# Optimization experiments

Measured on AMD Instinct MI355X. Metric: run time of the kernel, lower is better.

Reference implementation:

```python
import math
import jax, jax.numpy as jnp
import numpy as np

EPS_ATTN = 1e-8
LN_EPS = 1e-5


def layer_norm(x, g, b):
    mu = jnp.mean(x, axis=-1, keepdims=True)
    var = jnp.var(x, axis=-1, keepdims=True)
    return (x - mu) * jax.lax.rsqrt(var + LN_EPS) * g + b


def setup_inputs() -> dict:
    key = jax.random.key(0)
    ks = jax.random.split(key, 12)
    b, n, dim = 8, 8192, 384
    emb = 384
    m = int(emb * 0.5)  # 192 random features
    s = 0.02
    x = jax.random.normal(ks[0], (b, n, dim), dtype=jnp.float32)
    # fixed random-feature matrix (orthogonal*sqrt(m) in torch; random gaussian suffices as a baseline param)
    w = jax.random.normal(ks[1], (m, emb), dtype=jnp.float32) * math.sqrt(m) / math.sqrt(emb)
    # linear weights stored as [in, out] (torch Linear applies x @ W.T + b)
    kqv_w = jax.random.normal(ks[2], (dim, 3 * emb), dtype=jnp.float32) * s
    kqv_b = jax.random.normal(ks[3], (3 * emb,), dtype=jnp.float32) * s
    proj_w = jax.random.normal(ks[4], (emb, emb), dtype=jnp.float32) * s
    proj_b = jax.random.normal(ks[5], (emb,), dtype=jnp.float32) * s
    ln1_g = 1.0 + jax.random.normal(ks[6], (dim,), dtype=jnp.float32) * s
    ln1_b = jax.random.normal(ks[7], (dim,), dtype=jnp.float32) * s
    ln2_g = 1.0 + jax.random.normal(ks[8], (emb,), dtype=jnp.float32) * s
    ln2_b = jax.random.normal(ks[9], (emb,), dtype=jnp.float32) * s
    mlp_w1 = jax.random.normal(ks[10], (emb, emb), dtype=jnp.float32) * s
    mlp_b1 = jnp.zeros((emb,), dtype=jnp.float32)
    mlp_w2 = jax.random.normal(ks[11], (emb, emb), dtype=jnp.float32) * s
    mlp_b2 = jnp.zeros((emb,), dtype=jnp.float32)
    return {"x": x, "w": w, "kqv_w": kqv_w, "kqv_b": kqv_b, "proj_w": proj_w,
            "proj_b": proj_b, "ln1_g": ln1_g, "ln1_b": ln1_b, "ln2_g": ln2_g,
            "ln2_b": ln2_b, "mlp_w1": mlp_w1, "mlp_b1": mlp_b1,
            "mlp_w2": mlp_w2, "mlp_b2": mlp_b2}


def prm_exp(x, w):
    # FAVOR+ positive random features: exp(w @ x - |x|^2/2) / sqrt(m)
    m = w.shape[0]
    xd = 0.5 * jnp.sum(x * x, axis=-1, keepdims=True)          # [b, t, 1]
    wtx = jnp.einsum('bti,mi->btm', x, w)                       # [b, t, m]
    return jnp.exp(wtx - xd) / math.sqrt(m)


def reference(x, w, kqv_w, kqv_b, proj_w, proj_b, ln1_g, ln1_b,
              ln2_g, ln2_b, mlp_w1, mlp_b1, mlp_w2, mlp_b2):
    emb = proj_w.shape[0]
    h = layer_norm(x, ln1_g, ln1_b)
    kqv = h @ kqv_w + kqv_b                                     # [b, n, 3*emb]
    k, q, v = jnp.split(kqv, 3, axis=-1)
    kp = prm_exp(k, w)                                          # [b, n, m]
    qp = prm_exp(q, w)                                          # [b, n, m]
    D = jnp.einsum('btm,bm->bt', qp, kp.sum(axis=1))[..., None] # [b, n, 1]
    kptv = jnp.einsum('btn,btm->bnm', v, kp)                    # [b, emb, m]
    y = jnp.einsum('btm,bnm->btn', qp, kptv) / (D + EPS_ATTN)   # [b, n, emb]
    y = v + (y @ proj_w + proj_b)                               # residual (dropout=0)
    h2 = layer_norm(y, ln2_g, ln2_b)
    mlp = jax.nn.gelu(h2 @ mlp_w1 + mlp_b1, approximate=False) @ mlp_w2 + mlp_b2
    return y + mlp
```

## Files before the change

### kernel.cpp

```cpp
#include <hip/hip_runtime.h>
#include <cstdint>
#include <cstddef>


typedef __attribute__((ext_vector_type(8))) short s16x8;
typedef __attribute__((ext_vector_type(4))) short s16x4;
typedef __attribute__((ext_vector_type(4))) float fx4;
typedef __attribute__((ext_vector_type(8))) float fx8;

__device__ __forceinline__ float bf2f(short s) {
  union { float f; unsigned u; } z; z.u = ((unsigned)(unsigned short)s) << 16; return z.f;
}
__device__ __forceinline__ short f2bf(float f) {
  union { float f; unsigned u; } z; z.f = f;
  unsigned u = z.u;
  u += 0x7fffu + ((u >> 16) & 1u);
  return (short)(u >> 16);
}

__device__ __forceinline__ void mfma_bf16(fx4& d, s16x8 a, s16x8 b) {
  asm("v_mfma_f32_16x16x32_bf16 %0, %1, %2, %0" : "+v"(d) : "v"(a), "v"(b));
}

enum : int { M_BIAS=1, M_EXP=2, M_DIV=4, M_RESID=8, M_GELU=16, M_TSTORE=32,
             M_BATCHBT=64, M_KQVT=128, M_RESIDT=256, M_F32OUT=512,
             M_XA=1024, M_DOTB=2048 };

template<int BM, int BN, int MODE>
__global__ __launch_bounds__(256)
void gemm_tn(const short* __restrict__ A, int lda,
             const short* __restrict__ Bt, int ldbt, long btStride,
             short* __restrict__ C, int ldc,
             int K,
             const float* __restrict__ bias,
             const float* __restrict__ rowvec, float escale,
             const short* __restrict__ resid, int ldr, int rcol,
             short* __restrict__ vt)
{
  constexpr int WM = BM / 2, WN = BN / 2, MR = WM / 16, NR = WN / 16;
  constexpr int AIT = BM * 8 / 256, BIT = BN * 8 / 256;
  __shared__ __align__(16) short Al[BM][64];
  __shared__ __align__(16) short Bl[BN][64];
  __shared__ float xdl[(MODE & (M_XA | M_DOTB)) ? BM : 1];

  const int tid = threadIdx.x;
  const int gx = gridDim.x;
  const int nwg = gx * gridDim.y;
  const int o = blockIdx.x + gx * blockIdx.y;
  const int swz = (o & 7) * (nwg >> 3) + (o >> 3);
  const int bx = swz % gx, by = swz / gx;
  const int row0 = by * BM, col0 = bx * BN;

  const short* Bt2 = (MODE & M_BATCHBT)
      ? Bt + (size_t)(row0 >> 13) * (size_t)btStride : Bt;
  const int w = tid >> 6, l = tid & 63;
  const int wr = w >> 1, wc = w & 1;
  const int lr = l & 15, lk = l >> 4;

  fx4 acc[MR][NR];
#pragma unroll
  for (int m = 0; m < MR; ++m)
#pragma unroll
    for (int n = 0; n < NR; ++n)
#pragma unroll
      for (int j = 0; j < 4; ++j) acc[m][n][j] = 0.0f;

  s16x8 areg[AIT], breg[BIT];
  float xacc[(MODE & (M_XA | M_DOTB)) ? AIT : 1];
#pragma unroll
  for (int i = 0; i < (int)(sizeof(xacc) / sizeof(float)); ++i) xacc[i] = 0.0f;

  auto loadA = [&](int kt) {
    const short* p = A + (size_t)row0 * lda + kt * 64;
#pragma unroll
    for (int i = 0; i < AIT; ++i) {
      int ch = i * 256 + tid;
      areg[i] = *(const s16x8*)(p + (size_t)(ch >> 3) * lda + ((ch & 7) * 8));
      if (MODE & M_XA) {
#pragma unroll
        for (int jj = 0; jj < 8; ++jj) { float f = bf2f(areg[i][jj]); xacc[i] += f * f; }
      }
      if (MODE & M_DOTB) {
        const float* dv = rowvec + (row0 >> 13) * 192 + kt * 64 + (ch & 7) * 8;
#pragma unroll
        for (int jj = 0; jj < 8; ++jj) xacc[i] += bf2f(areg[i][jj]) * dv[jj];
      }
    }
  };
  auto loadB = [&](int kt) {
    const short* p = Bt2 + (size_t)col0 * ldbt + kt * 64;
#pragma unroll
    for (int i = 0; i < BIT; ++i) {
      int ch = i * 256 + tid;
      breg[i] = *(const s16x8*)(p + (size_t)(ch >> 3) * ldbt + ((ch & 7) * 8));
    }
  };
  auto storeA = [&]() {
#pragma unroll
    for (int i = 0; i < AIT; ++i) {
      int ch = i * 256 + tid, row = ch >> 3;
      *(s16x8*)&Al[row][((ch ^ row) & 7) * 8] = areg[i];
    }
  };
  auto storeB = [&]() {
#pragma unroll
    for (int i = 0; i < BIT; ++i) {
      int ch = i * 256 + tid, row = ch >> 3;
      *(s16x8*)&Bl[row][((ch ^ row) & 7) * 8] = breg[i];
    }
  };

  const int NT = K / 64;
  loadA(0); loadB(0); storeA(); storeB();
  __syncthreads();
  for (int kt = 0; kt < NT; ++kt) {
    if (kt + 1 < NT) { loadA(kt + 1); loadB(kt + 1); }
#pragma unroll
    for (int kk = 0; kk < 2; ++kk) {
      s16x8 af[MR], bfr[NR];
#pragma unroll
      for (int m = 0; m < MR; ++m) {
        const int ar = wr * WM + m * 16 + lr;
        af[m] = *(const s16x8*)&Al[ar][(((kk * 4 + lk) ^ ar) & 7) * 8];
      }
#pragma unroll
      for (int n = 0; n < NR; ++n) {
        const int br = wc * WN + n * 16 + lr;
        bfr[n] = *(const s16x8*)&Bl[br][(((kk * 4 + lk) ^ br) & 7) * 8];
      }
#pragma unroll
      for (int m = 0; m < MR; ++m)
#pragma unroll
        for (int n = 0; n < NR; ++n)
          mfma_bf16(acc[m][n], af[m], bfr[n]);
    }
    if (kt + 1 < NT) {
      __syncthreads();
      storeA(); storeB();
      __syncthreads();
    }
  }

  if (MODE & (M_XA | M_DOTB)) {
#pragma unroll
    for (int i = 0; i < (int)(sizeof(xacc) / sizeof(float)); ++i) {
      float s = xacc[i];
      s += __shfl_xor(s, 1); s += __shfl_xor(s, 2); s += __shfl_xor(s, 4);
      if ((tid & 7) == 0) xdl[i * 32 + (tid >> 3)] = (MODE & M_XA) ? 0.5f * s : s;
    }
    __syncthreads();
  }

#pragma unroll
  for (int m = 0; m < MR; ++m) {
#pragma unroll
    for (int n = 0; n < NR; ++n) {
      const int gcol = col0 + wc * WN + n * 16 + lr;
      const float bv = (MODE & M_BIAS) ? bias[gcol] : 0.0f;
#pragma unroll
      for (int j = 0; j < 4; ++j) {
        const int lrow = wr * WM + m * 16 + lk * 4 + j;
        const int grow = row0 + lrow;
        float v = acc[m][n][j] + bv;
        if (MODE & M_EXP)  v = expf(v - xdl[lrow]) * escale;
        if (MODE & M_DIV)  v = v / (xdl[lrow] + 1e-8f);
        if (MODE & M_GELU) v = 0.5f * v * (1.0f + erff(v * 0.70710678118654752f));
        if (MODE & M_RESID)  v += bf2f(resid[(size_t)grow * ldr + rcol + gcol]);
        if (MODE & M_RESIDT) v += bf2f(resid[((size_t)((grow >> 13) * ldr + gcol)) * 8192 + (grow & 8191)]);
        if (MODE & M_F32OUT) {
          ((float*)C)[(size_t)grow * ldc + gcol] = v;
        } else if (MODE & M_TSTORE) {
          C[((size_t)((grow >> 13) * ldc + gcol)) * 8192 + (grow & 8191)] = f2bf(v);
        } else if (MODE & M_KQVT) {
          if (gcol < 768) C[(size_t)grow * 768 + gcol] = f2bf(v);
          else vt[((size_t)((grow >> 13) * 384 + (gcol - 768))) * 8192 + (grow & 8191)] = f2bf(v);
        } else {
          C[(size_t)grow * ldc + gcol] = f2bf(v);
        }
      }
    }
  }
}

__global__ __launch_bounds__(256)
void gemm_kptv(const short* __restrict__ vT, const short* __restrict__ kpT,
               float* __restrict__ part)
{
  __shared__ __align__(16) short Al[128][64];
  __shared__ __align__(16) short Bl[64][64];
  const int tid = threadIdx.x;
  const int b = blockIdx.z >> 3, s = blockIdx.z & 7;
  const int row0 = blockIdx.x * 128, col0 = blockIdx.y * 64;
  const short* A  = vT  + ((size_t)(b * 384 + row0)) * 8192 + s * 1024;
  const short* Bt = kpT + ((size_t)(b * 192 + col0)) * 8192 + s * 1024;
  const int w = tid >> 6, l = tid & 63;
  const int wr = w >> 1, wc = w & 1, lr = l & 15, lk = l >> 4;

  fx4 acc[4][2];
#pragma unroll
  for (int m = 0; m < 4; ++m)
#pragma unroll
    for (int n = 0; n < 2; ++n)
#pragma unroll
      for (int j = 0; j < 4; ++j) acc[m][n][j] = 0.0f;

  s16x8 areg[4], breg[2];
  auto loadA = [&](int kt) {
#pragma unroll
    for (int i = 0; i < 4; ++i) {
      int ch = i * 256 + tid;
      areg[i] = *(const s16x8*)(A + kt * 64 + (size_t)(ch >> 3) * 8192 + ((ch & 7) * 8));
    }
  };
  auto loadB = [&](int kt) {
#pragma unroll
    for (int i = 0; i < 2; ++i) {
      int ch = i * 256 + tid;
      breg[i] = *(const s16x8*)(Bt + kt * 64 + (size_t)(ch >> 3) * 8192 + ((ch & 7) * 8));
    }
  };
  auto storeA = [&]() {
#pragma unroll
    for (int i = 0; i < 4; ++i) {
      int ch = i * 256 + tid, row = ch >> 3;
      *(s16x8*)&Al[row][((ch ^ row) & 7) * 8] = areg[i];
    }
  };
  auto storeB = [&]() {
#pragma unroll
    for (int i = 0; i < 2; ++i) {
      int ch = i * 256 + tid, row = ch >> 3;
      *(s16x8*)&Bl[row][((ch ^ row) & 7) * 8] = breg[i];
    }
  };

  loadA(0); loadB(0); storeA(); storeB();
  __syncthreads();
  for (int kt = 0; kt < 16; ++kt) {
    if (kt + 1 < 16) { loadA(kt + 1); loadB(kt + 1); }
#pragma unroll
    for (int kk = 0; kk < 2; ++kk) {
      s16x8 af[4], bfr[2];
#pragma unroll
      for (int m = 0; m < 4; ++m) {
        const int ar = wr * 64 + m * 16 + lr;
        af[m] = *(const s16x8*)&Al[ar][(((kk * 4 + lk) ^ ar) & 7) * 8];
      }
#pragma unroll
      for (int n = 0; n < 2; ++n) {
        const int br = wc * 32 + n * 16 + lr;
        bfr[n] = *(const s16x8*)&Bl[br][(((kk * 4 + lk) ^ br) & 7) * 8];
      }
#pragma unroll
      for (int m = 0; m < 4; ++m)
#pragma unroll
        for (int n = 0; n < 2; ++n)
          mfma_bf16(acc[m][n], af[m], bfr[n]);
    }
    if (kt + 1 < 16) {
      __syncthreads();
      storeA(); storeB();
      __syncthreads();
    }
  }

  float* outp = part + (size_t)blockIdx.z * 73728;
#pragma unroll
  for (int m = 0; m < 4; ++m)
#pragma unroll
    for (int n = 0; n < 2; ++n) {
      const int gm = col0 + wc * 32 + n * 16 + lr;
#pragma unroll
      for (int j = 0; j < 4; ++j) {
        const int gn = row0 + wr * 64 + m * 16 + lk * 4 + j;
        outp[(size_t)gn * 192 + gm] = acc[m][n][j];
      }
    }
}

__global__ void kptv_reduce(const float* __restrict__ part, short* __restrict__ outb)
{
  const int i = blockIdx.x * 256 + threadIdx.x;
  const int b = i / 73728, j = i - b * 73728;
  const float* p = part + (size_t)b * 8 * 73728 + j;
  float s = 0.0f;
#pragma unroll
  for (int k = 0; k < 8; ++k) s += p[(size_t)k * 73728];
  outb[i] = f2bf(s);
}

template<typename T>
__global__ __launch_bounds__(256)
void ln_kernel(const T* __restrict__ in, const float* __restrict__ g,
               const float* __restrict__ bta, short* __restrict__ out)
{
  const int tid = threadIdx.x, w = tid >> 6, l = tid & 63;
  const size_t t = (size_t)blockIdx.x * 4 + w;
  float x[8]; float sum = 0.0f, ss = 0.0f;
  const bool act = l < 48;
  if (act) {
    if constexpr (sizeof(T) == 2) {
      s16x8 v = *(const s16x8*)((const short*)in + t * 384 + l * 8);
#pragma unroll
      for (int i = 0; i < 8; ++i) x[i] = bf2f(v[i]);
    } else {
      fx8 v = *(const fx8*)((const float*)in + t * 384 + l * 8);
#pragma unroll
      for (int i = 0; i < 8; ++i) x[i] = v[i];
    }
#pragma unroll
    for (int i = 0; i < 8; ++i) { sum += x[i]; ss += x[i] * x[i]; }
  }
#pragma unroll
  for (int d = 1; d < 64; d <<= 1) { sum += __shfl_xor(sum, d); ss += __shfl_xor(ss, d); }
  const float mu = sum * (1.0f / 384.0f);
  const float rs = rsqrtf(ss * (1.0f / 384.0f) - mu * mu + 1e-5f);
  if (act) {
    fx8 gv = *(const fx8*)(g + l * 8);
    fx8 bv = *(const fx8*)(bta + l * 8);
    s16x8 o;
#pragma unroll
    for (int i = 0; i < 8; ++i) o[i] = f2bf((x[i] - mu) * rs * gv[i] + bv[i]);
    *(s16x8*)(out + t * 384 + l * 8) = o;
  }
}

__global__ __launch_bounds__(256)
void rowsum_kernel(const short* __restrict__ kpT, float* __restrict__ sum)
{
  const int tid = threadIdx.x;
  const short* row = kpT + (size_t)blockIdx.x * 8192;
  float s = 0.0f;
  for (int i = tid; i < 1024; i += 256) {
    s16x8 v = ((const s16x8*)row)[i];
#pragma unroll
    for (int k = 0; k < 8; ++k) s += bf2f(v[k]);
  }
#pragma unroll
  for (int d = 1; d < 64; d <<= 1) s += __shfl_xor(s, d);
  __shared__ float ps[4];
  if ((tid & 63) == 0) ps[tid >> 6] = s;
  __syncthreads();
  if (tid == 0) sum[blockIdx.x] = ps[0] + ps[1] + ps[2] + ps[3];
}

__global__ void transpose_kernel(const float* __restrict__ src, short* __restrict__ dst,
                                 int R, int Cc)
{
  __shared__ float tile[32][33];
  const int c0 = blockIdx.x * 32, r0 = blockIdx.y * 32;
  for (int i = threadIdx.y; i < 32; i += 8)
    tile[i][threadIdx.x] = src[(size_t)(r0 + i) * Cc + c0 + threadIdx.x];
  __syncthreads();
  for (int i = threadIdx.y; i < 32; i += 8)
    dst[(size_t)(c0 + i) * R + r0 + threadIdx.x] = f2bf(tile[threadIdx.x][i]);
}

__global__ void convert_kernel(const float* __restrict__ src, short* __restrict__ dst)
{
  const int i = blockIdx.x * 1024 + threadIdx.x * 4;
  fx4 v = *(const fx4*)(src + i);
  s16x4 o;
#pragma unroll
  for (int k = 0; k < 4; ++k) o[k] = f2bf(v[k]);
  *(s16x4*)(dst + i) = o;
}

extern "C" void kernel_launch(void* const* d_in, const int* in_sizes, int n_in,
                              void* d_out, int out_size, void* d_ws, size_t ws_size,
                              hipStream_t stream)
{
  const float* x      = (const float*)d_in[0];
  const float* w      = (const float*)d_in[1];
  const float* kqv_w  = (const float*)d_in[2];
  const float* kqv_b  = (const float*)d_in[3];
  const float* proj_w = (const float*)d_in[4];
  const float* proj_b = (const float*)d_in[5];
  const float* ln1_g  = (const float*)d_in[6];
  const float* ln1_b  = (const float*)d_in[7];
  const float* ln2_g  = (const float*)d_in[8];
  const float* ln2_b  = (const float*)d_in[9];
  const float* w1     = (const float*)d_in[10];
  const float* b1     = (const float*)d_in[11];
  const float* w2     = (const float*)d_in[12];
  const float* b2     = (const float*)d_in[13];

  char* p = (char*)d_ws;
  auto take = [&](size_t n) { char* r = p; p += (n + 255) & ~(size_t)255; return r; };
  short* wtKQV  = (short*)take(1152 * 384 * 2);
  short* wtPROJ = (short*)take(384 * 384 * 2);
  short* wtM1   = (short*)take(384 * 384 * 2);
  short* wtM2   = (short*)take(384 * 384 * 2);
  short* wB     = (short*)take(192 * 384 * 2);
  short* KQ     = (short*)take((size_t)65536 * 768 * 2);
  short* VT     = (short*)take((size_t)8 * 384 * 8192 * 2);
  char*  KPQ    = take(50331648);
  float* KPSUM = (float*)take(1536 * 4);
  float* KPART = (float*)take((size_t)64 * 73728 * 4);
  short* KPTVB = (short*)take(1179648);

  short* H   = (short*)KPQ;
  short* KPT = (short*)KPQ;
  short* QP  = (short*)(KPQ + 25165824);
  short* Y   = (short*)KPQ;
  short* YA  = KQ;
  short* G   = KQ;
  short* H2  = VT;

  const float ESC = 0.07216878364870323f;
  dim3 blk(256);

  transpose_kernel<<<dim3(36, 12), dim3(32, 8), 0, stream>>>(kqv_w, wtKQV, 384, 1152);
  transpose_kernel<<<dim3(12, 12), dim3(32, 8), 0, stream>>>(proj_w, wtPROJ, 384, 384);
  transpose_kernel<<<dim3(12, 12), dim3(32, 8), 0, stream>>>(w1, wtM1, 384, 384);
  transpose_kernel<<<dim3(12, 12), dim3(32, 8), 0, stream>>>(w2, wtM2, 384, 384);
  convert_kernel<<<72, blk, 0, stream>>>(w, wB);

  ln_kernel<float><<<16384, blk, 0, stream>>>(x, ln1_g, ln1_b, H);

  gemm_tn<128, 128, M_BIAS | M_KQVT><<<dim3(9, 512), blk, 0, stream>>>(
      H, 384, wtKQV, 384, 0, KQ, 768, 384, kqv_b, nullptr, 0.f, nullptr, 0, 0, VT);

  gemm_tn<128, 64, M_EXP | M_TSTORE | M_XA><<<dim3(3, 512), blk, 0, stream>>>(
      KQ, 768, wB, 384, 0, KPT, 192, 384, nullptr, nullptr, ESC, nullptr, 0, 0, nullptr);
  gemm_tn<128, 64, M_EXP | M_XA><<<dim3(3, 512), blk, 0, stream>>>(
      KQ + 384, 768, wB, 384, 0, QP, 192, 384, nullptr, nullptr, ESC, nullptr, 0, 0, nullptr);

  rowsum_kernel<<<1536, blk, 0, stream>>>(KPT, KPSUM);

  gemm_kptv<<<dim3(3, 3, 64), blk, 0, stream>>>(VT, KPT, KPART);
  kptv_reduce<<<2304, blk, 0, stream>>>(KPART, KPTVB);

  gemm_tn<128, 128, M_DIV | M_BATCHBT | M_DOTB><<<dim3(3, 512), blk, 0, stream>>>(
      QP, 192, KPTVB, 192, 73728, YA, 384, 192, nullptr, KPSUM, 0.f, nullptr, 0, 0, nullptr);

  gemm_tn<128, 128, M_BIAS | M_RESIDT><<<dim3(3, 512), blk, 0, stream>>>(
      YA, 384, wtPROJ, 384, 0, Y, 384, 384, proj_b, nullptr, 0.f, VT, 384, 0, nullptr);

  ln_kernel<short><<<16384, blk, 0, stream>>>(Y, ln2_g, ln2_b, H2);

  gemm_tn<128, 128, M_BIAS | M_GELU><<<dim3(3, 512), blk, 0, stream>>>(
      H2, 384, wtM1, 384, 0, G, 384, 384, b1, nullptr, 0.f, nullptr, 0, 0, nullptr);

  gemm_tn<128, 128, M_BIAS | M_RESID | M_F32OUT><<<dim3(3, 512), blk, 0, stream>>>(
      G, 384, wtM2, 384, 0, (short*)d_out, 384, 384, b2, nullptr, 0.f, Y, 384, 0, nullptr);
}
```

Baseline: 486.4 us.

## Use direct global-to-LDS async loads with double-buffered tiles in GEMMs

Adds an async mode to the tiled GEMM that uses global_load_lds to copy A/B tiles straight from global memory into double-buffered LDS, with the XOR swizzle moved to the global address side. This drops the register staging and the extra barrier-bounded store phase, so the next tile's load can overlap the current tile's MFMA work with one barrier per K step. It is enabled for the KQV, projection and two MLP GEMMs. It doubles LDS use per block, which may lower occupancy, and it relies on the barrier also waiting for the outstanding LDS-direct loads.

```diff
diff --git a/kernel.cpp b/kernel.cpp
--- a/kernel.cpp
+++ b/kernel.cpp
@@ -22,9 +22,15 @@
   asm("v_mfma_f32_16x16x32_bf16 %0, %1, %2, %0" : "+v"(d) : "v"(a), "v"(b));
 }
 
+__device__ __forceinline__ void gload_lds16(const short* src, short* lds) {
+  __builtin_amdgcn_global_load_lds(
+      (const __attribute__((address_space(1))) unsigned int*)src,
+      (__attribute__((address_space(3))) unsigned int*)lds, 16, 0, 0);
+}
+
 enum : int { M_BIAS=1, M_EXP=2, M_DIV=4, M_RESID=8, M_GELU=16, M_TSTORE=32,
              M_BATCHBT=64, M_KQVT=128, M_RESIDT=256, M_F32OUT=512,
-             M_XA=1024, M_DOTB=2048 };
+             M_XA=1024, M_DOTB=2048, M_ASYNC=4096 };
 
 template<int BM, int BN, int MODE>
 __global__ __launch_bounds__(256)
@@ -37,10 +43,12 @@
              const short* __restrict__ resid, int ldr, int rcol,
              short* __restrict__ vt)
 {
+  constexpr bool ASYNC = (MODE & M_ASYNC) != 0;
+  constexpr int NB = ASYNC ? 2 : 1;
   constexpr int WM = BM / 2, WN = BN / 2, MR = WM / 16, NR = WN / 16;
   constexpr int AIT = BM * 8 / 256, BIT = BN * 8 / 256;
-  __shared__ __align__(16) short Al[BM][64];
-  __shared__ __align__(16) short Bl[BN][64];
+  __shared__ __align__(16) short Al[NB][BM][64];
+  __shared__ __align__(16) short Bl[NB][BN][64];
   __shared__ float xdl[(MODE & (M_XA | M_DOTB)) ? BM : 1];
 
   const int tid = threadIdx.x;
@@ -99,34 +107,59 @@
 #pragma unroll
     for (int i = 0; i < AIT; ++i) {
       int ch = i * 256 + tid, row = ch >> 3;
-      *(s16x8*)&Al[row][((ch ^ row) & 7) * 8] = areg[i];
+      *(s16x8*)&Al[0][row][((ch ^ row) & 7) * 8] = areg[i];
     }
   };
   auto storeB = [&]() {
 #pragma unroll
     for (int i = 0; i < BIT; ++i) {
       int ch = i * 256 + tid, row = ch >> 3;
-      *(s16x8*)&Bl[row][((ch ^ row) & 7) * 8] = breg[i];
+      *(s16x8*)&Bl[0][row][((ch ^ row) & 7) * 8] = breg[i];
+    }
+  };
+
+  auto stageA = [&](int buf, int kt) {
+    const short* pb = A + (size_t)row0 * lda + kt * 64;
+#pragma unroll
+    for (int i = 0; i < AIT; ++i) {
+      int ch = i * 256 + tid, row = ch >> 3, c = ch & 7;
+      gload_lds16(pb + (size_t)row * lda + ((c ^ row) & 7) * 8,
+                  (short*)Al + (size_t)buf * BM * 64 + ch * 8);
+    }
+  };
+  auto stageB = [&](int buf, int kt) {
+    const short* pb = Bt2 + (size_t)col0 * ldbt + kt * 64;
+#pragma unroll
+    for (int i = 0; i < BIT; ++i) {
+      int ch = i * 256 + tid, row = ch >> 3, c = ch & 7;
+      gload_lds16(pb + (size_t)row * ldbt + ((c ^ row) & 7) * 8,
+                  (short*)Bl + (size_t)buf * BN * 64 + ch * 8);
     }
   };
 
   const int NT = K / 64;
-  loadA(0); loadB(0); storeA(); storeB();
+  int buf = 0;
+  if constexpr (ASYNC) { stageA(0, 0); stageB(0, 0); }
+  else { loadA(0); loadB(0); storeA(); storeB(); }
   __syncthreads();
   for (int kt = 0; kt < NT; ++kt) {
-    if (kt + 1 < NT) { loadA(kt + 1); loadB(kt + 1); }
+    if constexpr (ASYNC) {
+      if (kt + 1 < NT) { stageA(buf ^ 1, kt + 1); stageB(buf ^ 1, kt + 1); }
+    } else {
+      if (kt + 1 < NT) { loadA(kt + 1); loadB(kt + 1); }
+    }
 #pragma unroll
     for (int kk = 0; kk < 2; ++kk) {
       s16x8 af[MR], bfr[NR];
 #pragma unroll
       for (int m = 0; m < MR; ++m) {
         const int ar = wr * WM + m * 16 + lr;
-        af[m] = *(const s16x8*)&Al[ar][(((kk * 4 + lk) ^ ar) & 7) * 8];
+        af[m] = *(const s16x8*)&Al[buf][ar][(((kk * 4 + lk) ^ ar) & 7) * 8];
       }
 #pragma unroll
       for (int n = 0; n < NR; ++n) {
         const int br = wc * WN + n * 16 + lr;
-        bfr[n] = *(const s16x8*)&Bl[br][(((kk * 4 + lk) ^ br) & 7) * 8];
+        bfr[n] = *(const s16x8*)&Bl[buf][br][(((kk * 4 + lk) ^ br) & 7) * 8];
       }
 #pragma unroll
       for (int m = 0; m < MR; ++m)
@@ -134,10 +167,15 @@
         for (int n = 0; n < NR; ++n)
           mfma_bf16(acc[m][n], af[m], bfr[n]);
     }
-    if (kt + 1 < NT) {
+    if constexpr (ASYNC) {
       __syncthreads();
-      storeA(); storeB();
-      __syncthreads();
+      buf ^= 1;
+    } else {
+      if (kt + 1 < NT) {
+        __syncthreads();
+        storeA(); storeB();
+        __syncthreads();
+      }
     }
   }
 
@@ -418,7 +456,7 @@
 
   ln_kernel<float><<<16384, blk, 0, stream>>>(x, ln1_g, ln1_b, H);
 
-  gemm_tn<128, 128, M_BIAS | M_KQVT><<<dim3(9, 512), blk, 0, stream>>>(
+  gemm_tn<128, 128, M_BIAS | M_KQVT | M_ASYNC><<<dim3(9, 512), blk, 0, stream>>>(
       H, 384, wtKQV, 384, 0, KQ, 768, 384, kqv_b, nullptr, 0.f, nullptr, 0, 0, VT);
 
   gemm_tn<128, 64, M_EXP | M_TSTORE | M_XA><<<dim3(3, 512), blk, 0, stream>>>(
@@ -434,14 +472,14 @@
   gemm_tn<128, 128, M_DIV | M_BATCHBT | M_DOTB><<<dim3(3, 512), blk, 0, stream>>>(
       QP, 192, KPTVB, 192, 73728, YA, 384, 192, nullptr, KPSUM, 0.f, nullptr, 0, 0, nullptr);
 
-  gemm_tn<128, 128, M_BIAS | M_RESIDT><<<dim3(3, 512), blk, 0, stream>>>(
+  gemm_tn<128, 128, M_BIAS | M_RESIDT | M_ASYNC><<<dim3(3, 512), blk, 0, stream>>>(
       YA, 384, wtPROJ, 384, 0, Y, 384, 384, proj_b, nullptr, 0.f, VT, 384, 0, nullptr);
 
   ln_kernel<short><<<16384, blk, 0, stream>>>(Y, ln2_g, ln2_b, H2);
 
-  gemm_tn<128, 128, M_BIAS | M_GELU><<<dim3(3, 512), blk, 0, stream>>>(
+  gemm_tn<128, 128, M_BIAS | M_GELU | M_ASYNC><<<dim3(3, 512), blk, 0, stream>>>(
       H2, 384, wtM1, 384, 0, G, 384, 384, b1, nullptr, 0.f, nullptr, 0, 0, nullptr);
 
-  gemm_tn<128, 128, M_BIAS | M_RESID | M_F32OUT><<<dim3(3, 512), blk, 0, stream>>>(
+  gemm_tn<128, 128, M_BIAS | M_RESID | M_F32OUT | M_ASYNC><<<dim3(3, 512), blk, 0, stream>>>(
       G, 384, wtM2, 384, 0, (short*)d_out, 384, 384, b2, nullptr, 0.f, Y, 384, 0, nullptr);
 }
```

After: 501.5 us. +3.1%, slower.

## Stage GEMM epilogue through shared memory for coalesced vectorized stores

Applied to the files above, without the earlier changes.

Replaces per-element scalar global stores in the GEMM epilogue with a staging pass through LDS. The LDS is reused via a union with the A/B tiles, with a swizzle for transposed outputs. Each half (or quarter for fp32 output) of the tile is written to LDS and then stored to global memory as 16-byte vectors, including the transposed layouts used for V and the kp/qp outputs. This removes the strided 2-byte writes, especially the transposed ones, at the cost of extra barriers and LDS traffic.

```diff
diff --git a/kernel.cpp b/kernel.cpp
--- a/kernel.cpp
+++ b/kernel.cpp
@@ -39,8 +39,13 @@
 {
   constexpr int WM = BM / 2, WN = BN / 2, MR = WM / 16, NR = WN / 16;
   constexpr int AIT = BM * 8 / 256, BIT = BN * 8 / 256;
-  __shared__ __align__(16) short Al[BM][64];
-  __shared__ __align__(16) short Bl[BN][64];
+  constexpr int PITCH = BN + 8;
+
+  __shared__ __align__(16) union UB {
+    struct { short Al[BM][64]; short Bl[BN][64]; } s;
+    short b16[64 * PITCH];
+    float b32[32 * PITCH];
+  } u;
   __shared__ float xdl[(MODE & (M_XA | M_DOTB)) ? BM : 1];
 
   const int tid = threadIdx.x;
@@ -99,14 +104,14 @@
 #pragma unroll
     for (int i = 0; i < AIT; ++i) {
       int ch = i * 256 + tid, row = ch >> 3;
-      *(s16x8*)&Al[row][((ch ^ row) & 7) * 8] = areg[i];
+      *(s16x8*)&u.s.Al[row][((ch ^ row) & 7) * 8] = areg[i];
     }
   };
   auto storeB = [&]() {
 #pragma unroll
     for (int i = 0; i < BIT; ++i) {
       int ch = i * 256 + tid, row = ch >> 3;
-      *(s16x8*)&Bl[row][((ch ^ row) & 7) * 8] = breg[i];
+      *(s16x8*)&u.s.Bl[row][((ch ^ row) & 7) * 8] = breg[i];
     }
   };
 
@@ -121,12 +126,12 @@
 #pragma unroll
       for (int m = 0; m < MR; ++m) {
         const int ar = wr * WM + m * 16 + lr;
-        af[m] = *(const s16x8*)&Al[ar][(((kk * 4 + lk) ^ ar) & 7) * 8];
+        af[m] = *(const s16x8*)&u.s.Al[ar][(((kk * 4 + lk) ^ ar) & 7) * 8];
       }
 #pragma unroll
       for (int n = 0; n < NR; ++n) {
         const int br = wc * WN + n * 16 + lr;
-        bfr[n] = *(const s16x8*)&Bl[br][(((kk * 4 + lk) ^ br) & 7) * 8];
+        bfr[n] = *(const s16x8*)&u.s.Bl[br][(((kk * 4 + lk) ^ br) & 7) * 8];
       }
 #pragma unroll
       for (int m = 0; m < MR; ++m)
@@ -142,6 +147,7 @@
   }
 
   if (MODE & (M_XA | M_DOTB)) {
+    __syncthreads();
 #pragma unroll
     for (int i = 0; i < (int)(sizeof(xacc) / sizeof(float)); ++i) {
       float s = xacc[i];
@@ -151,32 +157,91 @@
     __syncthreads();
   }
 
-#pragma unroll
-  for (int m = 0; m < MR; ++m) {
-#pragma unroll
-    for (int n = 0; n < NR; ++n) {
-      const int gcol = col0 + wc * WN + n * 16 + lr;
-      const float bv = (MODE & M_BIAS) ? bias[gcol] : 0.0f;
-#pragma unroll
-      for (int j = 0; j < 4; ++j) {
-        const int lrow = wr * WM + m * 16 + lk * 4 + j;
-        const int grow = row0 + lrow;
-        float v = acc[m][n][j] + bv;
-        if (MODE & M_EXP)  v = expf(v - xdl[lrow]) * escale;
-        if (MODE & M_DIV)  v = v / (xdl[lrow] + 1e-8f);
-        if (MODE & M_GELU) v = 0.5f * v * (1.0f + erff(v * 0.70710678118654752f));
-        if (MODE & M_RESID)  v += bf2f(resid[(size_t)grow * ldr + rcol + gcol]);
-        if (MODE & M_RESIDT) v += bf2f(resid[((size_t)((grow >> 13) * ldr + gcol)) * 8192 + (grow & 8191)]);
-        if (MODE & M_F32OUT) {
-          ((float*)C)[(size_t)grow * ldc + gcol] = v;
-        } else if (MODE & M_TSTORE) {
-          C[((size_t)((grow >> 13) * ldc + gcol)) * 8192 + (grow & 8191)] = f2bf(v);
-        } else if (MODE & M_KQVT) {
-          if (gcol < 768) C[(size_t)grow * 768 + gcol] = f2bf(v);
-          else vt[((size_t)((grow >> 13) * 384 + (gcol - 768))) * 8192 + (grow & 8191)] = f2bf(v);
-        } else {
-          C[(size_t)grow * ldc + gcol] = f2bf(v);
+  auto val = [&](int m, int n, int j) -> float {
+    const int gcol = col0 + wc * WN + n * 16 + lr;
+    const int lrow = wr * WM + m * 16 + lk * 4 + j;
+    const int grow = row0 + lrow;
+    float v = acc[m][n][j] + ((MODE & M_BIAS) ? bias[gcol] : 0.0f);
+    if (MODE & M_EXP)  v = expf(v - xdl[lrow]) * escale;
+    if (MODE & M_DIV)  v = v / (xdl[lrow] + 1e-8f);
+    if (MODE & M_GELU) v = 0.5f * v * (1.0f + erff(v * 0.70710678118654752f));
+    if (MODE & M_RESID)  v += bf2f(resid[(size_t)grow * ldr + rcol + gcol]);
+    if (MODE & M_RESIDT) v += bf2f(resid[((size_t)((grow >> 13) * ldr + gcol)) * 8192 + (grow & 8191)]);
+    return v;
+  };
+
+  if constexpr (!(MODE & M_F32OUT)) {
+    const bool tst = (MODE & M_TSTORE) || ((MODE & M_KQVT) && col0 >= 768);
+    const int bb = row0 >> 13;
+    const int tb0 = row0 & 8191;
+#pragma unroll
+    for (int p = 0; p < 2; ++p) {
+      __syncthreads();
+      if (wr == p) {
+#pragma unroll
+        for (int m = 0; m < MR; ++m)
+#pragma unroll
+          for (int n = 0; n < NR; ++n)
+#pragma unroll
+            for (int j = 0; j < 4; ++j) {
+              const int rl = m * 16 + lk * 4 + j;
+              int c = wc * WN + n * 16 + lr;
+              if (tst) c ^= ((rl >> 3) & 7) << 3;
+              u.b16[rl * PITCH + c] = f2bf(val(m, n, j));
+            }
+      }
+      __syncthreads();
+      if (!tst) {
+        constexpr int CH = BN / 8;
+#pragma unroll
+        for (int i = 0; i < 64 * CH / 256; ++i) {
+          const int uu = i * 256 + tid, row = uu / CH, ch = uu % CH;
+          s16x8 vv = *(const s16x8*)&u.b16[row * PITCH + ch * 8];
+          *(s16x8*)(C + (size_t)(row0 + p * 64 + row) * ldc + col0 + ch * 8) = vv;
         }
+      } else {
+#pragma unroll
+        for (int i = 0; i < BN * 8 / 256; ++i) {
+          const int uu = i * 256 + tid, c = uu >> 3, rc = uu & 7;
+          s16x8 vv;
+#pragma unroll
+          for (int k = 0; k < 8; ++k) {
+            const int rl = rc * 8 + k;
+            vv[k] = u.b16[rl * PITCH + (c ^ ((((rl) >> 3) & 7) << 3))];
+          }
+          const size_t rowsel = (MODE & M_TSTORE)
+              ? (size_t)(bb * ldc + col0 + c)
+              : (size_t)(bb * 384 + (col0 - 768) + c);
+          short* dst = ((MODE & M_TSTORE) ? C : vt) + rowsel * 8192 + tb0 + p * 64 + rc * 8;
+          *(s16x8*)dst = vv;
+        }
+      }
+    }
+  } else {
+#pragma unroll
+    for (int p = 0; p < 4; ++p) {
+      __syncthreads();
+      if (wr == (p >> 1)) {
+#pragma unroll
+        for (int mm = 0; mm < 2; ++mm) {
+          const int m = (p & 1) * 2 + mm;
+#pragma unroll
+          for (int n = 0; n < NR; ++n)
+#pragma unroll
+            for (int j = 0; j < 4; ++j)
+              u.b32[(mm * 16 + lk * 4 + j) * PITCH + wc * WN + n * 16 + lr] = val(m, n, j);
+        }
+      }
+      __syncthreads();
+      constexpr int CH = BN / 8;
+#pragma unroll
+      for (int i = 0; i < 32 * CH / 256; ++i) {
+        const int uu = i * 256 + tid, row = uu / CH, ch = uu % CH;
+        fx4 v0 = *(const fx4*)&u.b32[row * PITCH + ch * 8];
+        fx4 v1 = *(const fx4*)&u.b32[row * PITCH + ch * 8 + 4];
+        float* dst = (float*)C + (size_t)(row0 + p * 32 + row) * ldc + col0 + ch * 8;
+        *(fx4*)dst = v0;
+        *(fx4*)(dst + 4) = v1;
       }
     }
   }
```

After: 426.3 us. -12.4%, faster.
